# Kernel optimization log

Hardware: AMD Instinct MI355X
Metric: run time of the kernel (lower is better)

Reference implementation:

```python
import jax, jax.numpy as jnp
import numpy as np

STRIDE = 32
ANCHOR_SCALES = (16, 32, 64)
RATIOS = (0.5, 1.0, 2.0)
BASE_SIZE = 16
A = 9                    # base_anchors
PRE_NMS_TOP_N = 6000
POST_NMS_TOP_N = 1000
NMS_THRESH = 0.7
MIN_SIZE = 16.0


def _base_anchors():
    w = h = float(BASE_SIZE)
    cx = cy = (BASE_SIZE - 1) * 0.5
    out = []
    for r in RATIOS:
        ws = np.round(np.sqrt(w * h / r))
        hs = np.round(ws * r)
        for s in ANCHOR_SCALES:
            W_, H_ = ws * s, hs * s
            out.append([cx - 0.5 * (W_ - 1), cy - 0.5 * (H_ - 1),
                        cx + 0.5 * (W_ - 1), cy + 0.5 * (H_ - 1)])
    return np.asarray(out, dtype=np.float32)  # [9,4]


def _conv(x, w, b, padding):
    y = jax.lax.conv_general_dilated(x, w, (1, 1), padding,
                                     dimension_numbers=('NCHW', 'OIHW', 'NCHW'))
    return y + b[None, :, None, None]


def reference(features, rpn_w, rpn_b, cls_w, cls_b, box_w, box_b, image_height, image_width):
    H, W = features.shape[2], features.shape[3]
    x = jax.nn.relu(_conv(features, rpn_w, rpn_b, 'SAME'))
    cls_score = _conv(x, cls_w, cls_b, 'VALID')           # [1,2A,H,W]
    cls_prob = jax.nn.softmax(cls_score, axis=1)           # nn.Softmax2d: softmax over all 2A channels
    bbox_pred = _conv(x, box_w, box_b, 'VALID')            # [1,4A,H,W]

    scores = cls_prob[0, A:].transpose(1, 2, 0).reshape(-1)       # fg scores [H*W*A]
    deltas = bbox_pred[0].transpose(1, 2, 0).reshape(-1, 4)        # [H*W*A,4]

    base = jnp.asarray(_base_anchors())
    sx = jnp.arange(W, dtype=jnp.float32) * STRIDE
    sy = jnp.arange(H, dtype=jnp.float32) * STRIDE
    sxx, syy = jnp.meshgrid(sx, sy)                                # [H,W]
    shifts = jnp.stack([sxx, syy, sxx, syy], axis=-1).reshape(-1, 4)
    anchors = (shifts[:, None, :] + base[None, :, :]).reshape(-1, 4)

    # bbox_transform_inv decode
    wa = anchors[:, 2] - anchors[:, 0] + 1.0
    ha = anchors[:, 3] - anchors[:, 1] + 1.0
    cxa = anchors[:, 0] + 0.5 * (wa - 1.0)
    cya = anchors[:, 1] + 0.5 * (ha - 1.0)
    cx = deltas[:, 0] * wa + cxa
    cy = deltas[:, 1] * ha + cya
    pw = wa * jnp.exp(deltas[:, 2])
    ph = ha * jnp.exp(deltas[:, 3])
    x1 = jnp.clip(cx - 0.5 * pw, 0.0, image_width - 1.0)
    y1 = jnp.clip(cy - 0.5 * ph, 0.0, image_height - 1.0)
    x2 = jnp.clip(cx + 0.5 * pw, 0.0, image_width - 1.0)
    y2 = jnp.clip(cy + 0.5 * ph, 0.0, image_height - 1.0)
    boxes = jnp.stack([x1, y1, x2, y2], axis=-1)

    valid0 = ((x2 - x1 + 1.0) >= MIN_SIZE) & ((y2 - y1 + 1.0) >= MIN_SIZE)
    scores = jnp.where(valid0, scores, -jnp.inf)

    top_scores, top_idx = jax.lax.top_k(scores, PRE_NMS_TOP_N)
    tb = boxes[top_idx]                                             # [P,4]
    tx1, ty1, tx2, ty2 = tb[:, 0], tb[:, 1], tb[:, 2], tb[:, 3]
    areas = (tx2 - tx1 + 1.0) * (ty2 - ty1 + 1.0)
    xx1 = jnp.maximum(tx1[:, None], tx1[None, :])
    yy1 = jnp.maximum(ty1[:, None], ty1[None, :])
    xx2 = jnp.minimum(tx2[:, None], tx2[None, :])
    yy2 = jnp.minimum(ty2[:, None], ty2[None, :])
    inter = jnp.maximum(xx2 - xx1 + 1.0, 0.0) * jnp.maximum(yy2 - yy1 + 1.0, 0.0)
    iou = inter / (areas[:, None] + areas[None, :] - inter)         # [P,P]

    def step(state, _):
        alive, = (state,) if not isinstance(state, tuple) else (None,)
        return state, None

    def nms_step(state, _):
        alive, sel_list = state
        s = jnp.where(alive, top_scores, -jnp.inf)
        j = jnp.argmax(s)
        ok = s[j] > -jnp.inf
        alive = alive & (jnp.take(iou, j, axis=0) <= NMS_THRESH)    # suppresses j too (iou=1)
        return (alive, sel_list), (j.astype(jnp.int32), ok)

    alive0 = jnp.isfinite(top_scores)
    (_, _), (sel, selv) = jax.lax.scan(nms_step, (alive0, 0),
                                       jnp.arange(POST_NMS_TOP_N), length=POST_NMS_TOP_N)

    out_boxes = tb[sel] * selv[:, None].astype(tb.dtype)            # zero-pad invalid slots
    rois = jnp.concatenate([jnp.zeros((POST_NMS_TOP_N, 1), tb.dtype), out_boxes], axis=1)
    return rois                                                     # [POST_NMS_TOP_N, 5]


def setup_inputs() -> dict:
    key = jax.random.key(0)
    ks = jax.random.split(key, 4)
    features = jax.random.normal(ks[0], (1, 256, 128, 128), dtype=jnp.float32)
    rpn_w = 0.01 * jax.random.normal(ks[1], (256, 256, 3, 3), dtype=jnp.float32)
    rpn_b = jnp.zeros((256,), jnp.float32)
    cls_w = 0.01 * jax.random.normal(ks[2], (18, 256, 1, 1), dtype=jnp.float32)
    cls_b = jnp.zeros((18,), jnp.float32)
    box_w = 0.01 * jax.random.normal(ks[3], (36, 256, 1, 1), dtype=jnp.float32)
    box_b = jnp.zeros((36,), jnp.float32)
    return {'features': features, 'rpn_w': rpn_w, 'rpn_b': rpn_b,
            'cls_w': cls_w, 'cls_b': cls_b, 'box_w': box_w, 'box_b': box_b,
            'image_height': 4096, 'image_width': 4096}
```

## Files before the change

### kernel.cpp

```cpp
#include <hip/hip_runtime.h>
#include <stdint.h>
#include <math.h>

typedef unsigned long long u64;
typedef unsigned int u32;
typedef float float4a __attribute__((ext_vector_type(4), aligned(4)));
typedef unsigned long long u64x2 __attribute__((ext_vector_type(2), aligned(16)));

static const size_t OFF_CTL   = 0;
static const size_t OFF_HIST  = 1024;
static const size_t OFF_DOTS  = 1049600;
static const size_t OFF_WCV   = 4588544;
static const size_t OFF_XD    = 6947840;
static const size_t OFF_BOX   = 23725056;
static const size_t OFF_KEYS  = 26084352;
static const size_t OFF_CKEY  = 27264000;
static const size_t OFF_CIDX  = 27313152;
static const size_t OFF_TB    = 27337728;
static const size_t OFF_ALIVE = 27458048;
static const size_t OFF_FPAD  = 32067584;
static const size_t OFF_MASKP = OFF_FPAD;

__device__ __forceinline__ float exp_xla(float x) {
    float m = floorf(__fmaf_rn(x, 1.44269504088896341f, 0.5f));
    float r = __fmaf_rn(m, -0.693359375f, x);
    r = __fmaf_rn(m, 2.12194440e-4f, r);
    float r2 = r * r;
    float p = 1.9875691500e-4f;
    p = __fmaf_rn(p, r, 1.3981999507e-3f);
    p = __fmaf_rn(p, r, 8.3334519073e-3f);
    p = __fmaf_rn(p, r, 4.1665795894e-2f);
    p = __fmaf_rn(p, r, 1.6666665459e-1f);
    p = __fmaf_rn(p, r, 5.0000001201e-1f);
    p = __fmaf_rn(p, r2, r);
    p = __fadd_rn(p, 1.0f);
    int mi = (int)m;
    return p * __int_as_float((mi + 127) << 23);
}

__device__ __forceinline__ void gload_lds16(const void* g, void* l) {
    __builtin_amdgcn_global_load_lds(
        (const __attribute__((address_space(1))) void*)g,
        (__attribute__((address_space(3))) void*)l, 16, 0, 0);
}

__global__ void prep_wcv(const float* __restrict__ rpn_w, float* __restrict__ wcv) {
    int t = blockIdx.x * 256 + threadIdx.x;
    if (t >= 589824) return;
    int tap = t / 65536, rem = t % 65536, ic = rem / 256, oc = rem % 256;
    wcv[t] = rpn_w[oc * 2304 + ic * 9 + tap];
}

__global__ void prep_pad(const float* __restrict__ feat, float* __restrict__ featP) {
    int t = blockIdx.x * 256 + threadIdx.x;
    if (t >= 256 * 130 * 132) return;
    int ic = t / 17160, rem = t % 17160, y = rem / 132, x = rem % 132;
    int sy = y - 1, sx = x - 1;
    float v = 0.f;
    if (sy >= 0 && sy < 128 && sx >= 0 && sx < 128)
        v = feat[ic * 16384 + sy * 128 + sx];
    featP[t] = v;
}

__global__ __launch_bounds__(256, 2) void conv3x3(const float* __restrict__ featP,
                                                  const float* __restrict__ wcv,
                                                  const float* __restrict__ rpn_b,
                                                  float* __restrict__ xd) {
    __shared__ float sW[8192];
    const int band = blockIdx.x & 7;
    const int slot = blockIdx.x >> 3;
    const int tx = slot & 7, ocb = slot >> 3;
    const int oc0 = ocb * 32;
    const int tid = threadIdx.x;
    const int wid = tid >> 6;
    const int lane = tid & 63;
    const int py = lane >> 2, px0 = (lane & 3) * 4;
    const int gy = band * 16 + py, gx0 = tx * 16 + px0;
    const int ocB = oc0 + wid * 8;
    float acc[4][8];
#pragma unroll
    for (int p = 0; p < 4; ++p)
#pragma unroll
        for (int o = 0; o < 8; ++o) acc[p][o] = 0.f;
#pragma unroll
    for (int tap = 0; tap < 9; ++tap) {
        __syncthreads();
        for (int idx = tid; idx < 8192; idx += 256)
            sW[idx] = wcv[tap * 65536 + (idx >> 5) * 256 + oc0 + (idx & 31)];
        __syncthreads();
        const float* fp = featP + (size_t)(gy + tap / 3) * 132 + (gx0 + tap % 3);
        const float* wl = sW + wid * 8;
#pragma unroll 4
        for (int ic = 0; ic < 256; ++ic) {
            float4a fA = *(const float4a*)(fp + (size_t)ic * 17160);
            float4a w0 = *(const float4a*)(wl + ic * 32);
            float4a w1 = *(const float4a*)(wl + ic * 32 + 4);
#pragma unroll
            for (int p = 0; p < 4; ++p) {
#pragma unroll
                for (int o = 0; o < 4; ++o)
                    acc[p][o] = __fmaf_rn(fA[p], w0[o], acc[p][o]);
#pragma unroll
                for (int o = 0; o < 4; ++o)
                    acc[p][4 + o] = __fmaf_rn(fA[p], w1[o], acc[p][4 + o]);
            }
        }
    }
#pragma unroll
    for (int p = 0; p < 4; ++p) {
        float* op = xd + (size_t)(gy * 128 + gx0 + p) * 256 + ocB;
#pragma unroll
        for (int o = 0; o < 8; ++o) {
            float v = __fadd_rn(acc[p][o], rpn_b[ocB + o]);
            op[o] = v > 0.f ? v : 0.f;
        }
    }
}

__global__ __launch_bounds__(256, 1) void heads_decode(const float* __restrict__ xd,
                                                       const float* __restrict__ cls_w,
                                                       const float* __restrict__ box_w,
                                                       const float* __restrict__ cls_b,
                                                       const float* __restrict__ box_b,
                                                       float4* __restrict__ boxes,
                                                       u64* __restrict__ keys) {
    __shared__ float sX[4][260];
    __shared__ float sD[4][54];
    const int tid = threadIdx.x;
    const int pix0 = blockIdx.x * 4;
    for (int idx = tid; idx < 1024; idx += 256)
        sX[idx >> 8][idx & 255] = xd[(size_t)(pix0 + (idx >> 8)) * 256 + (idx & 255)];
    __syncthreads();
    if (tid < 216) {
        const int pl = tid / 54, o = tid % 54;
        const float* wr = (o < 18) ? (cls_w + o * 256) : (box_w + (o - 18) * 256);
        const float4* x4 = (const float4*)&sX[pl][0];
        const float4* w4 = (const float4*)wr;
        float acc = 0.f;
        for (int q = 0; q < 64; ++q) {
            float4 xv = x4[q];
            float4 wv = w4[q];
            acc = __fmaf_rn(xv.x, wv.x, acc);
            acc = __fmaf_rn(xv.y, wv.y, acc);
            acc = __fmaf_rn(xv.z, wv.z, acc);
            acc = __fmaf_rn(xv.w, wv.w, acc);
        }
        sD[pl][o] = acc;
    }
    __syncthreads();
    if (tid >= 36) return;
    const int pl = tid / 9, a = tid % 9;
    const int pix = pix0 + pl;
    const float* dt = sD[pl];
    float d[54];
#pragma unroll
    for (int i = 0; i < 54; ++i)
        d[i] = __fadd_rn(dt[i], (i < 18 ? cls_b[i] : box_b[i - 18]));
    float m = d[0];
#pragma unroll
    for (int i = 1; i < 18; ++i) m = fmaxf(m, d[i]);
    float e[18];
#pragma unroll
    for (int i = 0; i < 18; ++i) e[i] = exp_xla(__fsub_rn(d[i], m));
    float s = e[0];
#pragma unroll
    for (int i = 1; i < 18; ++i) s = __fadd_rn(s, e[i]);
    const int y = pix >> 7, x = pix & 127;
    const float shx = (float)(x * 32), shy = (float)(y * 32);
    const float AW[9] = {368.f, 736.f, 1472.f, 256.f, 512.f, 1024.f, 176.f, 352.f, 704.f};
    const float AH[9] = {192.f, 384.f, 768.f, 256.f, 512.f, 1024.f, 352.f, 704.f, 1408.f};
    float score = e[9 + a] / s;
    float wa = AW[a], ha = AH[a];
    float cxa = __fadd_rn(shx, 7.5f), cya = __fadd_rn(shy, 7.5f);
    float dx = d[18 + 4 * a], dyy = d[19 + 4 * a];
    float dw = d[20 + 4 * a], dh = d[21 + 4 * a];
    float cx = __fadd_rn(__fmul_rn(dx, wa), cxa);
    float cy = __fadd_rn(__fmul_rn(dyy, ha), cya);
    float pw = __fmul_rn(wa, exp_xla(dw));
    float ph = __fmul_rn(ha, exp_xla(dh));
    float hx = __fmul_rn(0.5f, pw), hy = __fmul_rn(0.5f, ph);
    float x1 = fminf(fmaxf(__fsub_rn(cx, hx), 0.f), 4095.f);
    float y1 = fminf(fmaxf(__fsub_rn(cy, hy), 0.f), 4095.f);
    float x2 = fminf(fmaxf(__fadd_rn(cx, hx), 0.f), 4095.f);
    float y2 = fminf(fmaxf(__fadd_rn(cy, hy), 0.f), 4095.f);
    float vw = __fadd_rn(__fsub_rn(x2, x1), 1.0f);
    float vh = __fadd_rn(__fsub_rn(y2, y1), 1.0f);
    bool valid = (vw >= 16.0f) && (vh >= 16.0f);
    int i = pix * 9 + a;
    boxes[i] = make_float4(x1, y1, x2, y2);
    u64 k;
    if (valid) {
        u32 b = __float_as_uint(score);
        k = ((u64)(u32)~(b | 0x80000000u) << 32) | (u32)i;
    } else {
        k = (0xFFFFFFFFULL << 32) | (u32)i;
    }
    keys[i] = k;
}

__global__ __launch_bounds__(256) void hist_scan(const u64* __restrict__ keys,
                                                 u32* __restrict__ ghist,
                                                 u64* pfx, u32* tgt,
                                                 u32* done, int pass) {
    __shared__ u32 lh[256];
    __shared__ u32 lastFlag;
    __shared__ u32 h[256];
    __shared__ u32 incl[256];
    const int t = threadIdx.x;
    lh[t] = 0;
    if (t == 0) lastFlag = 0;
    __syncthreads();
    const u64 pref = *pfx;
    const u32 target0 = (pass == 0) ? 6000u : *tgt;
    const int shift = 56 - 8 * pass;
    for (int i = blockIdx.x * 256 + t; i < 147456; i += 64 * 256) {
        u64 k = keys[i];
        bool match = (pass == 0) || ((k >> (shift + 8)) == pref);
        if (match) atomicAdd(&lh[(u32)(k >> shift) & 0xFFu], 1u);
    }
    __syncthreads();
    if (lh[t]) atomicAdd(&ghist[t], lh[t]);
    __threadfence();
    __syncthreads();
    if (t == 0) {
        u32 prev = atomicAdd(done, 1u);
        if (prev == 63) lastFlag = 1;
    }
    __syncthreads();
    if (!lastFlag) return;
    u32 hv = atomicAdd(&ghist[t], 0u);
    h[t] = hv;
    incl[t] = hv;
    __syncthreads();
    for (int off = 1; off < 256; off <<= 1) {
        u32 v = (t >= off) ? incl[t - off] : 0u;
        __syncthreads();
        incl[t] += v;
        __syncthreads();
    }
    u64 p0 = (pass == 0) ? 0ULL : pref;
    u32 before = incl[t] - h[t];
    if (before < target0 && target0 <= incl[t]) {
        *pfx = (p0 << 8) | (u64)t;
        *tgt = target0 - before;
    }
}

__global__ void compact(const u64* __restrict__ keys, const u64* __restrict__ kstar,
                        u32* count, u64* __restrict__ ckey, u32* __restrict__ cidx,
                        u64* __restrict__ alive0) {
    if (blockIdx.x == 0 && threadIdx.x < 128) alive0[threadIdx.x] = 0ULL;
    int i = blockIdx.x * 256 + threadIdx.x;
    if (i >= 147456) return;
    u64 k = keys[i];
    if ((k >> 32) <= *kstar) {
        u32 pos = atomicAdd(count, 1u);
        if (pos < 6144) { ckey[pos] = k; cidx[pos] = (u32)(k & 0xFFFFFFFFu); }
    }
}

__global__ __launch_bounds__(256) void rank_scatter(const u64* __restrict__ ckey,
                                                    const u32* __restrict__ cidx,
                                                    const u32* __restrict__ count,
                                                    const float4* __restrict__ boxes,
                                                    float4* __restrict__ tb,
                                                    u64* __restrict__ alive0) {
    __shared__ u64 LK[6144];
    int N = (int)*count; if (N > 6144) N = 6144;
    for (int i = threadIdx.x; i < N; i += 256) LK[i] = ckey[i];
    __syncthreads();
    int e = blockIdx.x * 256 + threadIdx.x;
    if (e >= N) return;
    u64 myK = LK[e];
    u32 myI = cidx[e];
    int rank = 0;
    for (int c = 0; c < N; ++c) rank += (LK[c] < myK);
    if (rank < 6000) {
        tb[rank] = boxes[myI];
        atomicOr(&alive0[rank >> 6], 1ULL << (rank & 63));
    }
}

__global__ __launch_bounds__(256) void nms_mask(const float4* __restrict__ tb,
                                                u64* __restrict__ mask) {
    int tid = blockIdx.x * 256 + threadIdx.x;
    if (tid >= 6000 * 94) return;
    int j = tid / 94, w = tid % 94;
    float4 bj = tb[j];
    float arJ = __fmul_rn(__fadd_rn(__fsub_rn(bj.z, bj.x), 1.0f),
                          __fadd_rn(__fsub_rn(bj.w, bj.y), 1.0f));
    u64 m = 0;
    int base = w * 64;
#pragma unroll 4
    for (int b = 0; b < 64; ++b) {
        int i = base + b;
        if (i >= 6000) break;
        float4 bi = tb[i];
        float arI = __fmul_rn(__fadd_rn(__fsub_rn(bi.z, bi.x), 1.0f),
                              __fadd_rn(__fsub_rn(bi.w, bi.y), 1.0f));
        float xx1 = fmaxf(bj.x, bi.x), yy1 = fmaxf(bj.y, bi.y);
        float xx2 = fminf(bj.z, bi.z), yy2 = fminf(bj.w, bi.w);
        float ww = fmaxf(__fadd_rn(__fsub_rn(xx2, xx1), 1.0f), 0.0f);
        float hh = fmaxf(__fadd_rn(__fsub_rn(yy2, yy1), 1.0f), 0.0f);
        float inter = __fmul_rn(ww, hh);
        float uni = __fsub_rn(__fadd_rn(arJ, arI), inter);
        float iou = inter / uni;
        if (iou > 0.7f) m |= (1ULL << b);
    }
    mask[(size_t)j * 128 + 2 * (w & 63) + (w >> 6)] = m;
}

__global__ __launch_bounds__(64, 1) void nms_seq(const u64* __restrict__ alive0,
                                                 const u64* __restrict__ mask,
                                                 const float4* __restrict__ tb,
                                                 float* __restrict__ out) {
    __shared__ __align__(16) u64 lwin[2][64 * 128];
    __shared__ u32 sel[1000];
    const int lane = threadIdx.x;
    u64 wl = alive0[lane];
    u64 wh = (lane < 30) ? alive0[64 + lane] : 0ULL;
    int base = -1000000;
    int pbase = -1;
    int cur = 0;
    int k = 0;
    for (; k < 1000; ++k) {
        int j;
        {
            u64 blo = __ballot(wl != 0ULL);
            if (blo) {
                int l = __ffsll((long long)blo) - 1;
                u32 a = __builtin_amdgcn_readlane((u32)wl, l);
                u32 b = __builtin_amdgcn_readlane((u32)(wl >> 32), l);
                u64 w = ((u64)b << 32) | (u64)a;
                j = l * 64 + __ffsll((long long)w) - 1;
            } else {
                u64 bhi = __ballot(wh != 0ULL);
                if (!bhi) break;
                int l = __ffsll((long long)bhi) - 1;
                u32 a = __builtin_amdgcn_readlane((u32)wh, l);
                u32 b = __builtin_amdgcn_readlane((u32)(wh >> 32), l);
                u64 w = ((u64)b << 32) | (u64)a;
                j = (64 + l) * 64 + __ffsll((long long)w) - 1;
            }
        }
        if (lane == 0) sel[k] = (u32)j;
        if (j >= base + 64) {
            if (pbase >= 0 && j < pbase + 64) {
                asm volatile("s_waitcnt vmcnt(0)" ::: "memory");
                cur ^= 1;
                base = pbase;
            } else {
                int js = (j > 5936) ? 5936 : j;
                asm volatile("s_waitcnt vmcnt(0)" ::: "memory");
                const char* gsrc = (const char*)mask + (size_t)js * 1024 + (size_t)lane * 16;
                char* ldst = (char*)&lwin[cur][0];
#pragma unroll
                for (int i = 0; i < 64; ++i)
                    gload_lds16(gsrc + (size_t)i * 1024, ldst + i * 1024);
                base = js;
                asm volatile("s_waitcnt vmcnt(0)" ::: "memory");
            }
            pbase = -1;
            if (base + 64 < 6000) {
                int ps = (base + 64 > 5936) ? 5936 : (base + 64);
                const char* gs2 = (const char*)mask + (size_t)ps * 1024 + (size_t)lane * 16;
                char* ld2 = (char*)&lwin[cur ^ 1][0];
#pragma unroll
                for (int i = 0; i < 64; ++i)
                    gload_lds16(gs2 + (size_t)i * 1024, ld2 + i * 1024);
                pbase = ps;
            }
        }
        const int s = j - base;
        u64x2 rd = *(const u64x2*)&lwin[cur][(size_t)s * 128 + 2 * lane];
        u64 rl = rd.x;
        u64 rh = rd.y;
        wl &= ~rl;
        if (lane < 30) wh &= ~rh;
    }
    __syncthreads();
    for (int r = lane; r < k; r += 64) {
        int j = (int)sel[r];
        float4 bj = tb[j];
        out[r * 5 + 1] = bj.x;
        out[r * 5 + 2] = bj.y;
        out[r * 5 + 3] = bj.z;
        out[r * 5 + 4] = bj.w;
    }
}

extern "C" void kernel_launch(void* const* d_in, const int* in_sizes, int n_in,
                              void* d_out, int out_size, void* d_ws, size_t ws_size,
                              hipStream_t stream) {
    const float *feat = nullptr, *rpn_w = nullptr, *rpn_b = nullptr;
    const float *cls_w = nullptr, *cls_b = nullptr, *box_w = nullptr, *box_b = nullptr;
    for (int i = 0; i < n_in; ++i) {
        switch (in_sizes[i]) {
            case 4194304: feat  = (const float*)d_in[i]; break;
            case 589824:  rpn_w = (const float*)d_in[i]; break;
            case 256:     rpn_b = (const float*)d_in[i]; break;
            case 4608:    cls_w = (const float*)d_in[i]; break;
            case 18:      cls_b = (const float*)d_in[i]; break;
            case 9216:    box_w = (const float*)d_in[i]; break;
            case 36:      box_b = (const float*)d_in[i]; break;
            default: break;
        }
    }

    char* w = (char*)d_ws;
    u64* pfx       = (u64*)(w + OFF_CTL);
    u32* tgt       = (u32*)(w + OFF_CTL + 8);
    u32* ctlCount  = (u32*)(w + OFF_CTL + 12);
    u32* done      = (u32*)(w + OFF_CTL + 16);
    u32* hist      = (u32*)(w + OFF_HIST);
    float* wcv     = (float*)(w + OFF_WCV);
    float* xd      = (float*)(w + OFF_XD);
    float4* boxes  = (float4*)(w + OFF_BOX);
    u64* keys      = (u64*)(w + OFF_KEYS);
    u64* ckey      = (u64*)(w + OFF_CKEY);
    u32* cidx      = (u32*)(w + OFF_CIDX);
    float4* tb     = (float4*)(w + OFF_TB);
    u64* alive0    = (u64*)(w + OFF_ALIVE);
    u64* maskP     = (u64*)(w + OFF_MASKP);
    float* featP   = (float*)(w + OFF_FPAD);

    hipMemsetAsync(d_ws, 0, OFF_HIST + 8 * 256 * 4, stream);
    hipMemsetAsync(d_out, 0, (size_t)out_size * sizeof(float), stream);

    prep_wcv<<<2304, 256, 0, stream>>>(rpn_w, wcv);
    prep_pad<<<17160, 256, 0, stream>>>(feat, featP);
    conv3x3<<<512, 256, 0, stream>>>(featP, wcv, rpn_b, xd);
    heads_decode<<<4096, 256, 0, stream>>>(xd, cls_w, box_w, cls_b, box_b, boxes, keys);
    for (int p = 0; p < 4; ++p)
        hist_scan<<<64, 256, 0, stream>>>(keys, hist + p * 256, pfx, tgt, done + p, p);
    compact<<<576, 256, 0, stream>>>(keys, pfx, ctlCount, ckey, cidx, alive0);
    rank_scatter<<<24, 256, 0, stream>>>(ckey, cidx, ctlCount, boxes, tb, alive0);
    nms_mask<<<2204, 256, 0, stream>>>(tb, maskP);
    nms_seq<<<1, 64, 0, stream>>>(alive0, maskP, tb, (float*)d_out);
}
```

Baseline: 888.2 us.

## Fuse prep kernels and merge radix-select passes with compaction via grid barrier

Merges the weight-transpose and padding prep kernels into one launch. Replaces four hist_scan launches plus the compact launch with a single 64-block persistent kernel that runs all radix passes behind a spin-wait grid barrier, then compacts. This removes roughly five kernel launches and their inter-kernel gaps. The cost is a software grid barrier that relies on all 64 blocks being co-resident, and a compaction that now runs on only 64 blocks.

Result: no change. 876.6 us (median of 2 runs) (-1.3%).

```diff
diff --git a/kernel.cpp b/kernel.cpp
--- a/kernel.cpp
+++ b/kernel.cpp
@@ -9,7 +9,6 @@
 
 static const size_t OFF_CTL   = 0;
 static const size_t OFF_HIST  = 1024;
-static const size_t OFF_DOTS  = 1049600;
 static const size_t OFF_WCV   = 4588544;
 static const size_t OFF_XD    = 6947840;
 static const size_t OFF_BOX   = 23725056;
@@ -44,22 +43,24 @@
         (__attribute__((address_space(3))) void*)l, 16, 0, 0);
 }
 
-__global__ void prep_wcv(const float* __restrict__ rpn_w, float* __restrict__ wcv) {
-    int t = blockIdx.x * 256 + threadIdx.x;
-    if (t >= 589824) return;
-    int tap = t / 65536, rem = t % 65536, ic = rem / 256, oc = rem % 256;
-    wcv[t] = rpn_w[oc * 2304 + ic * 9 + tap];
-}
-
-__global__ void prep_pad(const float* __restrict__ feat, float* __restrict__ featP) {
-    int t = blockIdx.x * 256 + threadIdx.x;
-    if (t >= 256 * 130 * 132) return;
-    int ic = t / 17160, rem = t % 17160, y = rem / 132, x = rem % 132;
-    int sy = y - 1, sx = x - 1;
-    float v = 0.f;
-    if (sy >= 0 && sy < 128 && sx >= 0 && sx < 128)
-        v = feat[ic * 16384 + sy * 128 + sx];
-    featP[t] = v;
+__global__ void prep_all(const float* __restrict__ rpn_w, float* __restrict__ wcv,
+                         const float* __restrict__ feat, float* __restrict__ featP) {
+    int b = blockIdx.x;
+    if (b < 2304) {
+        int t = b * 256 + threadIdx.x;
+        if (t >= 589824) return;
+        int tap = t / 65536, rem = t % 65536, ic = rem / 256, oc = rem % 256;
+        wcv[t] = rpn_w[oc * 2304 + ic * 9 + tap];
+    } else {
+        int t = (b - 2304) * 256 + threadIdx.x;
+        if (t >= 256 * 130 * 132) return;
+        int ic = t / 17160, rem = t % 17160, y = rem / 132, x = rem % 132;
+        int sy = y - 1, sx = x - 1;
+        float v = 0.f;
+        if (sy >= 0 && sy < 128 && sx >= 0 && sx < 128)
+            v = feat[ic * 16384 + sy * 128 + sx];
+        featP[t] = v;
+    }
 }
 
 __global__ __launch_bounds__(256, 2) void conv3x3(const float* __restrict__ featP,
@@ -198,64 +199,61 @@
     keys[i] = k;
 }
 
-__global__ __launch_bounds__(256) void hist_scan(const u64* __restrict__ keys,
-                                                 u32* __restrict__ ghist,
-                                                 u64* pfx, u32* tgt,
-                                                 u32* done, int pass) {
+__global__ __launch_bounds__(256) void radix_compact(const u64* __restrict__ keys,
+                                                     u32* __restrict__ ghist,
+                                                     u32* done, u32* count,
+                                                     u64* __restrict__ ckey,
+                                                     u32* __restrict__ cidx,
+                                                     u64* __restrict__ alive0) {
     __shared__ u32 lh[256];
-    __shared__ u32 lastFlag;
-    __shared__ u32 h[256];
+    __shared__ u32 sh[256];
     __shared__ u32 incl[256];
+    __shared__ u32 bdig, btgt;
     const int t = threadIdx.x;
-    lh[t] = 0;
-    if (t == 0) lastFlag = 0;
-    __syncthreads();
-    const u64 pref = *pfx;
-    const u32 target0 = (pass == 0) ? 6000u : *tgt;
-    const int shift = 56 - 8 * pass;
+    if (blockIdx.x == 0 && t < 128) alive0[t] = 0ULL;
+    u64 pref = 0;
+    u32 target = 6000;
+    for (int pass = 0; pass < 4; ++pass) {
+        lh[t] = 0;
+        __syncthreads();
+        const int shift = 56 - 8 * pass;
+        for (int i = blockIdx.x * 256 + t; i < 147456; i += 64 * 256) {
+            u64 k = keys[i];
+            bool match = (pass == 0) || ((k >> (shift + 8)) == pref);
+            if (match) atomicAdd(&lh[(u32)(k >> shift) & 0xFFu], 1u);
+        }
+        __syncthreads();
+        if (lh[t]) atomicAdd(&ghist[pass * 256 + t], lh[t]);
+        __threadfence();
+        __syncthreads();
+        if (t == 0) {
+            atomicAdd(done, 1u);
+            const u32 need = 64u * (u32)(pass + 1);
+            while (atomicAdd(done, 0u) < need) { }
+        }
+        __syncthreads();
+        u32 hv = atomicAdd(&ghist[pass * 256 + t], 0u);
+        sh[t] = hv;
+        incl[t] = hv;
+        __syncthreads();
+        for (int off = 1; off < 256; off <<= 1) {
+            u32 v = (t >= off) ? incl[t - off] : 0u;
+            __syncthreads();
+            incl[t] += v;
+            __syncthreads();
+        }
+        u32 before = incl[t] - sh[t];
+        if (before < target && target <= incl[t]) { bdig = (u32)t; btgt = target - before; }
+        __syncthreads();
+        pref = (pref << 8) | (u64)bdig;
+        target = btgt;
+    }
     for (int i = blockIdx.x * 256 + t; i < 147456; i += 64 * 256) {
         u64 k = keys[i];
-        bool match = (pass == 0) || ((k >> (shift + 8)) == pref);
-        if (match) atomicAdd(&lh[(u32)(k >> shift) & 0xFFu], 1u);
-    }
-    __syncthreads();
-    if (lh[t]) atomicAdd(&ghist[t], lh[t]);
-    __threadfence();
-    __syncthreads();
-    if (t == 0) {
-        u32 prev = atomicAdd(done, 1u);
-        if (prev == 63) lastFlag = 1;
-    }
-    __syncthreads();
-    if (!lastFlag) return;
-    u32 hv = atomicAdd(&ghist[t], 0u);
-    h[t] = hv;
-    incl[t] = hv;
-    __syncthreads();
-    for (int off = 1; off < 256; off <<= 1) {
-        u32 v = (t >= off) ? incl[t - off] : 0u;
-        __syncthreads();
-        incl[t] += v;
-        __syncthreads();
-    }
-    u64 p0 = (pass == 0) ? 0ULL : pref;
-    u32 before = incl[t] - h[t];
-    if (before < target0 && target0 <= incl[t]) {
-        *pfx = (p0 << 8) | (u64)t;
-        *tgt = target0 - before;
-    }
-}
-
-__global__ void compact(const u64* __restrict__ keys, const u64* __restrict__ kstar,
-                        u32* count, u64* __restrict__ ckey, u32* __restrict__ cidx,
-                        u64* __restrict__ alive0) {
-    if (blockIdx.x == 0 && threadIdx.x < 128) alive0[threadIdx.x] = 0ULL;
-    int i = blockIdx.x * 256 + threadIdx.x;
-    if (i >= 147456) return;
-    u64 k = keys[i];
-    if ((k >> 32) <= *kstar) {
-        u32 pos = atomicAdd(count, 1u);
-        if (pos < 6144) { ckey[pos] = k; cidx[pos] = (u32)(k & 0xFFFFFFFFu); }
+        if ((k >> 32) <= pref) {
+            u32 pos = atomicAdd(count, 1u);
+            if (pos < 6144) { ckey[pos] = k; cidx[pos] = (u32)(k & 0xFFFFFFFFu); }
+        }
     }
 }
 
@@ -408,8 +406,6 @@
     }
 
     char* w = (char*)d_ws;
-    u64* pfx       = (u64*)(w + OFF_CTL);
-    u32* tgt       = (u32*)(w + OFF_CTL + 8);
     u32* ctlCount  = (u32*)(w + OFF_CTL + 12);
     u32* done      = (u32*)(w + OFF_CTL + 16);
     u32* hist      = (u32*)(w + OFF_HIST);
@@ -427,13 +423,10 @@
     hipMemsetAsync(d_ws, 0, OFF_HIST + 8 * 256 * 4, stream);
     hipMemsetAsync(d_out, 0, (size_t)out_size * sizeof(float), stream);
 
-    prep_wcv<<<2304, 256, 0, stream>>>(rpn_w, wcv);
-    prep_pad<<<17160, 256, 0, stream>>>(feat, featP);
+    prep_all<<<2304 + 17160, 256, 0, stream>>>(rpn_w, wcv, feat, featP);
     conv3x3<<<512, 256, 0, stream>>>(featP, wcv, rpn_b, xd);
     heads_decode<<<4096, 256, 0, stream>>>(xd, cls_w, box_w, cls_b, box_b, boxes, keys);
-    for (int p = 0; p < 4; ++p)
-        hist_scan<<<64, 256, 0, stream>>>(keys, hist + p * 256, pfx, tgt, done + p, p);
-    compact<<<576, 256, 0, stream>>>(keys, pfx, ctlCount, ckey, cidx, alive0);
+    radix_compact<<<64, 256, 0, stream>>>(keys, hist, done, ctlCount, ckey, cidx, alive0);
     rank_scatter<<<24, 256, 0, stream>>>(ckey, cidx, ctlCount, boxes, tb, alive0);
     nms_mask<<<2204, 256, 0, stream>>>(tb, maskP);
     nms_seq<<<1, 64, 0, stream>>>(alive0, maskP, tb, (float*)d_out);
```
